# Performance work log

Measured on AMD Instinct MI355X. Metric: run time of the kernel, lower is better.

The kernel has to match this reference:

```python
import jax, jax.numpy as jnp
import numpy as np

IN_FEATURES = 1024
OUT_FEATURES = 1024
NNZ = 104858  # round(0.1 * 1024 * 1024)
BATCH = 1024


def setup_inputs() -> dict:
    key = jax.random.key(0)
    k1, k2, k3, k4 = jax.random.split(key, 4)
    x = jax.random.normal(k1, (BATCH, IN_FEATURES), dtype=jnp.float32)
    weights = jax.random.normal(k2, (NNZ,), dtype=jnp.float32)
    bias = jax.random.normal(k3, (OUT_FEATURES,), dtype=jnp.float32)
    # COO indices: row in [0, OUT_FEATURES), col in [0, IN_FEATURES)
    indices = jax.random.randint(k4, (2, NNZ), 0, 1024, dtype=jnp.int64)
    return {"x": x, "weights": weights, "bias": bias, "indices": indices}


def reference(x, weights, bias, indices):
    # y[n, r] = sum_{k: row_k == r} w_k * x[n, col_k]  (unstructured COO spmm)
    row, col = indices[0], indices[1]
    # gather input columns per nnz entry: [nnz, N]
    gathered = x.T[col] * weights[:, None]
    # scatter-add into output rows: [out_features, N]
    out = jax.ops.segment_sum(gathered, row, num_segments=OUT_FEATURES)
    return out.T + bias  # [N, out_features]
```

## Files before the change

kernel.cpp:

```cpp
#include <hip/hip_runtime.h>
#include <hip/hip_bf16.h>

#define NNZ   104858
#define NB    1024
#define NIN   1024
#define NOUT  1024

typedef __bf16 bf16;
typedef bf16  bf16x8 __attribute__((ext_vector_type(8)));
typedef float f32x4  __attribute__((ext_vector_type(4)));

__global__ __launch_bounds__(256)
void k_pre(const float* __restrict__ x, float* __restrict__ Wd,
           bf16* __restrict__ xb) {
    const int b = blockIdx.x, t = threadIdx.x;
    if (b < 512) {
        float4 z = {0.f, 0.f, 0.f, 0.f};
        float4* w4 = (float4*)Wd;
        int i = (b * 256 + t) * 2;
        w4[i] = z; w4[i + 1] = z;
    } else {
        const int base = ((b - 512) * 256 + t) * 8;
        const float4* s4 = (const float4*)(x + base);
        float4 v0 = s4[0], v1 = s4[1];
        bf16x8 o;
        o[0] = (bf16)v0.x; o[1] = (bf16)v0.y; o[2] = (bf16)v0.z; o[3] = (bf16)v0.w;
        o[4] = (bf16)v1.x; o[5] = (bf16)v1.y; o[6] = (bf16)v1.z; o[7] = (bf16)v1.w;
        *(bf16x8*)(xb + base) = o;
    }
}

__global__ __launch_bounds__(256)
void k_densify(const int* __restrict__ idx, const float* __restrict__ w,
               float* __restrict__ Wd) {
    int k = blockIdx.x * 256 + threadIdx.x;
    if (k < NNZ) {
        int r = idx[k] & (NOUT - 1);
        int c = idx[NNZ + k] & (NIN - 1);
        atomicAdd(&Wd[r * NIN + c], w[k]);
    }
}

__global__ __launch_bounds__(256)
void k_convW(const float* __restrict__ Wd, bf16* __restrict__ wb) {
    const int base = (blockIdx.x * 256 + threadIdx.x) * 8;
    const float4* s4 = (const float4*)(Wd + base);
    float4 v0 = s4[0], v1 = s4[1];
    bf16x8 o;
    o[0] = (bf16)v0.x; o[1] = (bf16)v0.y; o[2] = (bf16)v0.z; o[3] = (bf16)v0.w;
    o[4] = (bf16)v1.x; o[5] = (bf16)v1.y; o[6] = (bf16)v1.z; o[7] = (bf16)v1.w;
    *(bf16x8*)(wb + base) = o;
}

__device__ __forceinline__ void gload_lds16(const void* g, void* l) {
    __builtin_amdgcn_global_load_lds((const __attribute__((address_space(1))) void*)g,
                                     (__attribute__((address_space(3))) void*)l,
                                     16, 0, 0);
}

__global__ __launch_bounds__(512)
void k_gemm(const bf16* __restrict__ A, const bf16* __restrict__ B,
            const float* __restrict__ bias, float* __restrict__ out) {
    __shared__ __align__(16) bf16 As[2][64 * 64];
    __shared__ __align__(16) bf16 Bs[2][64 * 64];
    __shared__ f32x4 red[4][64][4];

    const int t  = threadIdx.x;
    const int m0 = blockIdx.x * 64, n0 = blockIdx.y * 64;
    const int lane = t & 63;
    const int wv = t >> 6;
    const int half = wv >> 2;
    const int w4 = wv & 3, wr = w4 >> 1, wc = w4 & 1;
    const int fr = lane & 15, fg = lane >> 4;

    const int th   = t & 255;
    const int srow = th >> 3;
    const int sg   = th & 7;

    f32x4 acc[2][2] = {};

    for (int ks = 0; ks < 8; ++ks) {
        const int kbase = half * 512 + ks * 64;
        #pragma unroll
        for (int i = 0; i < 2; ++i) {
            int row = i * 32 + srow;
            int g2  = sg ^ (row & 7);
            gload_lds16(A + (size_t)(m0 + row) * NIN + kbase + g2 * 8,
                        As[half] + row * 64 + sg * 8);
            gload_lds16(B + (size_t)(n0 + row) * NIN + kbase + g2 * 8,
                        Bs[half] + row * 64 + sg * 8);
        }
        __syncthreads();

        bf16x8 af[2][2], bfr[2][2];
        #pragma unroll
        for (int mi = 0; mi < 2; ++mi) {
            int row = wr * 32 + mi * 16 + fr;
            #pragma unroll
            for (int kk = 0; kk < 2; ++kk) {
                int gsw = (kk * 4 + fg) ^ (row & 7);
                af[mi][kk] = *(const bf16x8*)(As[half] + row * 64 + gsw * 8);
            }
        }
        #pragma unroll
        for (int ni = 0; ni < 2; ++ni) {
            int row = wc * 32 + ni * 16 + fr;
            #pragma unroll
            for (int kk = 0; kk < 2; ++kk) {
                int gsw = (kk * 4 + fg) ^ (row & 7);
                bfr[ni][kk] = *(const bf16x8*)(Bs[half] + row * 64 + gsw * 8);
            }
        }
        #pragma unroll
        for (int mi = 0; mi < 2; ++mi)
            #pragma unroll
            for (int ni = 0; ni < 2; ++ni)
                #pragma unroll
                for (int kk = 0; kk < 2; ++kk)
                    acc[mi][ni] = __builtin_amdgcn_mfma_f32_16x16x32_bf16(
                        af[mi][kk], bfr[ni][kk], acc[mi][ni], 0, 0, 0);
        __syncthreads();
    }

    if (half == 1) {
        #pragma unroll
        for (int mi = 0; mi < 2; ++mi)
            #pragma unroll
            for (int ni = 0; ni < 2; ++ni)
                red[w4][lane][mi * 2 + ni] = acc[mi][ni];
    }
    __syncthreads();
    if (half == 0) {
        #pragma unroll
        for (int mi = 0; mi < 2; ++mi) {
            #pragma unroll
            for (int ni = 0; ni < 2; ++ni) {
                f32x4 p = red[w4][lane][mi * 2 + ni];
                int row0 = m0 + wr * 32 + mi * 16 + fg * 4;
                int col  = n0 + wc * 32 + ni * 16 + fr;
                float bb = bias[col];
                #pragma unroll
                for (int j = 0; j < 4; ++j)
                    out[(size_t)(row0 + j) * NOUT + col] = acc[mi][ni][j] + p[j] + bb;
            }
        }
    }
}

static inline size_t align256(size_t v) { return (v + 255) & ~(size_t)255; }

extern "C" void kernel_launch(void* const* d_in, const int* in_sizes, int n_in,
                              void* d_out, int out_size, void* d_ws, size_t ws_size,
                              hipStream_t stream) {
    const float* x    = (const float*)d_in[0];
    const float* wts  = (const float*)d_in[1];
    const float* bias = (const float*)d_in[2];
    const int*   idx  = (const int*)d_in[3];

    char* ws = (char*)d_ws;
    size_t off = 0;
    float* Wd = (float*)(ws + off); off = align256(off + (size_t)NOUT * NIN * 4);
    bf16*  xb = (bf16*) (ws + off); off = align256(off + (size_t)NB * NIN * 2);
    bf16*  wb = (bf16*) (ws + off); off = align256(off + (size_t)NOUT * NIN * 2);

    const int nb_nnz = (NNZ + 255) / 256;

    k_pre<<<1024, 256, 0, stream>>>(x, Wd, xb);
    k_densify<<<nb_nnz, 256, 0, stream>>>(idx, wts, Wd);
    k_convW<<<512, 256, 0, stream>>>(Wd, wb);
    k_gemm<<<dim3(16, 16), 512, 0, stream>>>(xb, wb, bias, (float*)d_out);
}
```

Baseline: 29.68 us.

## Fuse weight fp32-to-bf16 conversion into GEMM B-tile loading and remap block order

Removes the separate conversion kernel that turned the densified fp32 weight matrix into bf16. The GEMM now loads fp32 weight rows into registers, converts them to bf16, and writes them into the swizzled LDS tile, prefetching the next k-slice after the barrier. It also switches to a 1D grid whose block-to-tile mapping groups blocks by XCD. This saves one launch and a full read/write pass over the weights. In exchange every GEMM block reads fp32 weights (twice the bytes) and issues register-staged LDS stores instead of direct global-to-LDS loads.

Result: faster. 29.02 us (median of 2 runs) (-2.2%).

```diff
diff --git a/kernel.cpp b/kernel.cpp
--- a/kernel.cpp
+++ b/kernel.cpp
@@ -41,17 +41,6 @@
     }
 }
 
-__global__ __launch_bounds__(256)
-void k_convW(const float* __restrict__ Wd, bf16* __restrict__ wb) {
-    const int base = (blockIdx.x * 256 + threadIdx.x) * 8;
-    const float4* s4 = (const float4*)(Wd + base);
-    float4 v0 = s4[0], v1 = s4[1];
-    bf16x8 o;
-    o[0] = (bf16)v0.x; o[1] = (bf16)v0.y; o[2] = (bf16)v0.z; o[3] = (bf16)v0.w;
-    o[4] = (bf16)v1.x; o[5] = (bf16)v1.y; o[6] = (bf16)v1.z; o[7] = (bf16)v1.w;
-    *(bf16x8*)(wb + base) = o;
-}
-
 __device__ __forceinline__ void gload_lds16(const void* g, void* l) {
     __builtin_amdgcn_global_load_lds((const __attribute__((address_space(1))) void*)g,
                                      (__attribute__((address_space(3))) void*)l,
@@ -59,25 +48,37 @@
 }
 
 __global__ __launch_bounds__(512)
-void k_gemm(const bf16* __restrict__ A, const bf16* __restrict__ B,
+void k_gemm(const bf16* __restrict__ A, const float* __restrict__ Wd,
             const float* __restrict__ bias, float* __restrict__ out) {
     __shared__ __align__(16) bf16 As[2][64 * 64];
     __shared__ __align__(16) bf16 Bs[2][64 * 64];
     __shared__ f32x4 red[4][64][4];
 
-    const int t  = threadIdx.x;
-    const int m0 = blockIdx.x * 64, n0 = blockIdx.y * 64;
+    const int b  = blockIdx.x;
+    const int id = (b & 7) * 32 + (b >> 3);
+    const int m0 = (id & 15) * 64, n0 = (id >> 4) * 64;
+
+    const int t    = threadIdx.x;
     const int lane = t & 63;
-    const int wv = t >> 6;
+    const int wv   = t >> 6;
     const int half = wv >> 2;
-    const int w4 = wv & 3, wr = w4 >> 1, wc = w4 & 1;
-    const int fr = lane & 15, fg = lane >> 4;
+    const int w4   = wv & 3, wr = w4 >> 1, wc = w4 & 1;
+    const int fr   = lane & 15, fg = lane >> 4;
 
     const int th   = t & 255;
     const int srow = th >> 3;
     const int sg   = th & 7;
+    const int brow = th >> 2;
+    const int bq   = th & 3;
 
     f32x4 acc[2][2] = {};
+
+    const float* wrow = Wd + (size_t)(n0 + brow) * NIN + half * 512;
+    float4 bv0, bv1, bv2, bv3;
+    {
+        const float4* p = (const float4*)(wrow + bq * 16);
+        bv0 = p[0]; bv1 = p[1]; bv2 = p[2]; bv3 = p[3];
+    }
 
     for (int ks = 0; ks < 8; ++ks) {
         const int kbase = half * 512 + ks * 64;
@@ -87,10 +88,24 @@
             int g2  = sg ^ (row & 7);
             gload_lds16(A + (size_t)(m0 + row) * NIN + kbase + g2 * 8,
                         As[half] + row * 64 + sg * 8);
-            gload_lds16(B + (size_t)(n0 + row) * NIN + kbase + g2 * 8,
-                        Bs[half] + row * 64 + sg * 8);
+        }
+        {
+            bf16x8 o0, o1;
+            o0[0] = (bf16)bv0.x; o0[1] = (bf16)bv0.y; o0[2] = (bf16)bv0.z; o0[3] = (bf16)bv0.w;
+            o0[4] = (bf16)bv1.x; o0[5] = (bf16)bv1.y; o0[6] = (bf16)bv1.z; o0[7] = (bf16)bv1.w;
+            o1[0] = (bf16)bv2.x; o1[1] = (bf16)bv2.y; o1[2] = (bf16)bv2.z; o1[3] = (bf16)bv2.w;
+            o1[4] = (bf16)bv3.x; o1[5] = (bf16)bv3.y; o1[6] = (bf16)bv3.z; o1[7] = (bf16)bv3.w;
+            int g0 = (bq * 2)     ^ (brow & 7);
+            int g1 = (bq * 2 + 1) ^ (brow & 7);
+            *(bf16x8*)(Bs[half] + brow * 64 + g0 * 8) = o0;
+            *(bf16x8*)(Bs[half] + brow * 64 + g1 * 8) = o1;
         }
         __syncthreads();
+
+        if (ks < 7) {
+            const float4* p = (const float4*)(wrow + (ks + 1) * 64 + bq * 16);
+            bv0 = p[0]; bv1 = p[1]; bv2 = p[2]; bv3 = p[3];
+        }
 
         bf16x8 af[2][2], bfr[2][2];
         #pragma unroll
@@ -161,12 +176,10 @@
     size_t off = 0;
     float* Wd = (float*)(ws + off); off = align256(off + (size_t)NOUT * NIN * 4);
     bf16*  xb = (bf16*) (ws + off); off = align256(off + (size_t)NB * NIN * 2);
-    bf16*  wb = (bf16*) (ws + off); off = align256(off + (size_t)NOUT * NIN * 2);
 
     const int nb_nnz = (NNZ + 255) / 256;
 
     k_pre<<<1024, 256, 0, stream>>>(x, Wd, xb);
     k_densify<<<nb_nnz, 256, 0, stream>>>(idx, wts, Wd);
-    k_convW<<<512, 256, 0, stream>>>(Wd, wb);
-    k_gemm<<<dim3(16, 16), 512, 0, stream>>>(xb, wb, bias, (float*)d_out);
+    k_gemm<<<256, 512, 0, stream>>>(xb, Wd, bias, (float*)d_out);
 }
```

## Fuse weight bf16 conversion into GEMM and switch to LDS-free 32x32 MFMA

Applied to the files above, without the earlier changes.

Drops the separate fp32-to-bf16 weight conversion kernel and converts the dense weight rows to bf16 inside the GEMM as they are loaded. The GEMM is rewritten as a direct-from-global 32x32x16 MFMA kernel with no shared memory and no split-K reduction, and tiles are assigned to blocks in an XCD-aware order so each die's L2 can reuse weight rows. This saves one launch and one round trip of the weight matrix through memory. In exchange the GEMM reads fp32 weights (twice the bytes) and gets less operand reuse because it no longer stages tiles in LDS.

Result: slower. 42.70 us (+43.9%).

```diff
diff --git a/kernel.cpp b/kernel.cpp
--- a/kernel.cpp
+++ b/kernel.cpp
@@ -7,8 +7,8 @@
 #define NOUT  1024
 
 typedef __bf16 bf16;
-typedef bf16  bf16x8 __attribute__((ext_vector_type(8)));
-typedef float f32x4  __attribute__((ext_vector_type(4)));
+typedef bf16  bf16x8  __attribute__((ext_vector_type(8)));
+typedef float f32x16  __attribute__((ext_vector_type(16)));
 
 __global__ __launch_bounds__(256)
 void k_pre(const float* __restrict__ x, float* __restrict__ Wd,
@@ -42,108 +42,43 @@
 }
 
 __global__ __launch_bounds__(256)
-void k_convW(const float* __restrict__ Wd, bf16* __restrict__ wb) {
-    const int base = (blockIdx.x * 256 + threadIdx.x) * 8;
-    const float4* s4 = (const float4*)(Wd + base);
-    float4 v0 = s4[0], v1 = s4[1];
-    bf16x8 o;
-    o[0] = (bf16)v0.x; o[1] = (bf16)v0.y; o[2] = (bf16)v0.z; o[3] = (bf16)v0.w;
-    o[4] = (bf16)v1.x; o[5] = (bf16)v1.y; o[6] = (bf16)v1.z; o[7] = (bf16)v1.w;
-    *(bf16x8*)(wb + base) = o;
-}
+void k_gemm(const bf16* __restrict__ A, const float* __restrict__ Wd,
+            const float* __restrict__ bias, float* __restrict__ out) {
+    const int b     = blockIdx.x;
+    const int xcd   = b & 7;
+    const int local = b >> 3;
+    const int ntile = xcd * 4 + (local & 3);
+    const int msup  = local >> 2;
+    const int wave  = threadIdx.x >> 6;
+    const int lane  = threadIdx.x & 63;
 
-__device__ __forceinline__ void gload_lds16(const void* g, void* l) {
-    __builtin_amdgcn_global_load_lds((const __attribute__((address_space(1))) void*)g,
-                                     (__attribute__((address_space(3))) void*)l,
-                                     16, 0, 0);
-}
+    const int m0 = msup * 128 + wave * 32;
+    const int n0 = ntile * 32;
+    const int lrow = lane & 31;
+    const int lk   = (lane >> 5) * 8;
 
-__global__ __launch_bounds__(512)
-void k_gemm(const bf16* __restrict__ A, const bf16* __restrict__ B,
-            const float* __restrict__ bias, float* __restrict__ out) {
-    __shared__ __align__(16) bf16 As[2][64 * 64];
-    __shared__ __align__(16) bf16 Bs[2][64 * 64];
-    __shared__ f32x4 red[4][64][4];
+    const bf16*  ap = A  + (size_t)(m0 + lrow) * NIN + lk;
+    const float* bp = Wd + (size_t)(n0 + lrow) * NIN + lk;
 
-    const int t  = threadIdx.x;
-    const int m0 = blockIdx.x * 64, n0 = blockIdx.y * 64;
-    const int lane = t & 63;
-    const int wv = t >> 6;
-    const int half = wv >> 2;
-    const int w4 = wv & 3, wr = w4 >> 1, wc = w4 & 1;
-    const int fr = lane & 15, fg = lane >> 4;
+    f32x16 acc = {};
 
-    const int th   = t & 255;
-    const int srow = th >> 3;
-    const int sg   = th & 7;
-
-    f32x4 acc[2][2] = {};
-
-    for (int ks = 0; ks < 8; ++ks) {
-        const int kbase = half * 512 + ks * 64;
-        #pragma unroll
-        for (int i = 0; i < 2; ++i) {
-            int row = i * 32 + srow;
-            int g2  = sg ^ (row & 7);
-            gload_lds16(A + (size_t)(m0 + row) * NIN + kbase + g2 * 8,
-                        As[half] + row * 64 + sg * 8);
-            gload_lds16(B + (size_t)(n0 + row) * NIN + kbase + g2 * 8,
-                        Bs[half] + row * 64 + sg * 8);
-        }
-        __syncthreads();
-
-        bf16x8 af[2][2], bfr[2][2];
-        #pragma unroll
-        for (int mi = 0; mi < 2; ++mi) {
-            int row = wr * 32 + mi * 16 + fr;
-            #pragma unroll
-            for (int kk = 0; kk < 2; ++kk) {
-                int gsw = (kk * 4 + fg) ^ (row & 7);
-                af[mi][kk] = *(const bf16x8*)(As[half] + row * 64 + gsw * 8);
-            }
-        }
-        #pragma unroll
-        for (int ni = 0; ni < 2; ++ni) {
-            int row = wc * 32 + ni * 16 + fr;
-            #pragma unroll
-            for (int kk = 0; kk < 2; ++kk) {
-                int gsw = (kk * 4 + fg) ^ (row & 7);
-                bfr[ni][kk] = *(const bf16x8*)(Bs[half] + row * 64 + gsw * 8);
-            }
-        }
-        #pragma unroll
-        for (int mi = 0; mi < 2; ++mi)
-            #pragma unroll
-            for (int ni = 0; ni < 2; ++ni)
-                #pragma unroll
-                for (int kk = 0; kk < 2; ++kk)
-                    acc[mi][ni] = __builtin_amdgcn_mfma_f32_16x16x32_bf16(
-                        af[mi][kk], bfr[ni][kk], acc[mi][ni], 0, 0, 0);
-        __syncthreads();
+    #pragma unroll 8
+    for (int ks = 0; ks < 64; ++ks) {
+        bf16x8 av = *(const bf16x8*)(ap + ks * 16);
+        float4 b0 = *(const float4*)(bp + ks * 16);
+        float4 b1 = *(const float4*)(bp + ks * 16 + 4);
+        bf16x8 bv;
+        bv[0] = (bf16)b0.x; bv[1] = (bf16)b0.y; bv[2] = (bf16)b0.z; bv[3] = (bf16)b0.w;
+        bv[4] = (bf16)b1.x; bv[5] = (bf16)b1.y; bv[6] = (bf16)b1.z; bv[7] = (bf16)b1.w;
+        acc = __builtin_amdgcn_mfma_f32_32x32x16_bf16(av, bv, acc, 0, 0, 0);
     }
 
-    if (half == 1) {
-        #pragma unroll
-        for (int mi = 0; mi < 2; ++mi)
-            #pragma unroll
-            for (int ni = 0; ni < 2; ++ni)
-                red[w4][lane][mi * 2 + ni] = acc[mi][ni];
-    }
-    __syncthreads();
-    if (half == 0) {
-        #pragma unroll
-        for (int mi = 0; mi < 2; ++mi) {
-            #pragma unroll
-            for (int ni = 0; ni < 2; ++ni) {
-                f32x4 p = red[w4][lane][mi * 2 + ni];
-                int row0 = m0 + wr * 32 + mi * 16 + fg * 4;
-                int col  = n0 + wc * 32 + ni * 16 + fr;
-                float bb = bias[col];
-                #pragma unroll
-                for (int j = 0; j < 4; ++j)
-                    out[(size_t)(row0 + j) * NOUT + col] = acc[mi][ni][j] + p[j] + bb;
-            }
-        }
+    const float bb = bias[n0 + lrow];
+    const int rbase = m0 + 4 * (lane >> 5);
+    #pragma unroll
+    for (int reg = 0; reg < 16; ++reg) {
+        int row = rbase + (reg & 3) + 8 * (reg >> 2);
+        out[(size_t)row * NOUT + n0 + lrow] = acc[reg] + bb;
     }
 }
 
@@ -161,12 +96,10 @@
     size_t off = 0;
     float* Wd = (float*)(ws + off); off = align256(off + (size_t)NOUT * NIN * 4);
     bf16*  xb = (bf16*) (ws + off); off = align256(off + (size_t)NB * NIN * 2);
-    bf16*  wb = (bf16*) (ws + off); off = align256(off + (size_t)NOUT * NIN * 2);
 
     const int nb_nnz = (NNZ + 255) / 256;
 
     k_pre<<<1024, 256, 0, stream>>>(x, Wd, xb);
     k_densify<<<nb_nnz, 256, 0, stream>>>(idx, wts, Wd);
-    k_convW<<<512, 256, 0, stream>>>(Wd, wb);
-    k_gemm<<<dim3(16, 16), 512, 0, stream>>>(xb, wb, bias, (float*)d_out);
+    k_gemm<<<256, 256, 0, stream>>>(xb, Wd, bias, (float*)d_out);
 }
```
